# Optimization experiments

Hardware: AMD Instinct MI355X
Metric: run time of the kernel (lower is better)

Reference implementation:

```python
import jax, jax.numpy as jnp
import numpy as np

H = W = 32
C = 384
NH = 12
HEAD = C // NH
SCALE = HEAD ** -0.5
WS = 8            # window size
SS = 4            # shift size
N = WS * WS       # tokens per window (64)
NW = (H // WS) * (W // WS)  # windows per image (16)
HIDDEN = 4 * C
EPS = 1e-5
SQRT_2_OVER_PI = float(np.sqrt(2.0 / np.pi))


def _relative_position_index():
    ch = np.arange(WS)
    coords = np.stack(np.meshgrid(ch, ch, indexing='ij')).reshape(2, -1)  # [2, N]
    rel = (coords[:, :, None] - coords[:, None, :]).transpose(1, 2, 0)    # [N, N, 2]
    rel[:, :, 0] += WS - 1
    rel[:, :, 1] += WS - 1
    rel[:, :, 0] *= 2 * WS - 1
    return rel.sum(-1)  # [N, N] int


def _attn_mask():
    img = np.zeros((H, W), np.float32)
    sl = (slice(0, -WS), slice(-WS, -SS), slice(-SS, None))
    cnt = 0
    for hs in sl:
        for ws_ in sl:
            img[hs, ws_] = cnt
            cnt += 1
    m = img.reshape(H // WS, WS, W // WS, WS).transpose(0, 2, 1, 3).reshape(-1, N)  # [nW, N]
    am = m[:, None, :] - m[:, :, None]
    return np.where(am != 0, -100.0, 0.0).astype(np.float32)  # [nW, N, N]


REL_IDX = jnp.asarray(_relative_position_index())
ATTN_MASK = jnp.asarray(_attn_mask())


def _gelu(x):
    return x * 0.5 * (1.0 + jnp.tanh(SQRT_2_OVER_PI * (x + 0.044715 * x ** 3)))


def _layernorm(x, g, b):
    mu = jnp.mean(x, axis=-1, keepdims=True)
    var = jnp.mean(jnp.square(x - mu), axis=-1, keepdims=True)
    return (x - mu) * jax.lax.rsqrt(var + EPS) * g + b


def _window_partition(x):  # [B,H,W,C] -> [B*nW, N, C]
    B = x.shape[0]
    x = x.reshape(B, H // WS, WS, W // WS, WS, C).transpose(0, 1, 3, 2, 4, 5)
    return x.reshape(-1, N, C)


def _window_reverse(w, B):  # [B*nW, N, C] -> [B,H,W,C]
    x = w.reshape(B, H // WS, W // WS, WS, WS, C).transpose(0, 1, 3, 2, 4, 5)
    return x.reshape(B, H, W, C)


def setup_inputs() -> dict:
    key = jax.random.key(0)
    ks = jax.random.split(key, 16)
    s = 0.02
    return {
        'x': jax.random.normal(ks[0], (32, H * W, C), jnp.float32),
        'norm1_g': jnp.ones((C,), jnp.float32),
        'norm1_b': jnp.zeros((C,), jnp.float32),
        'qkv_w': jax.random.normal(ks[1], (C, 3 * C), jnp.float32) * s,
        'qkv_b': jnp.zeros((3 * C,), jnp.float32),
        'rel_bias_table': jax.random.normal(ks[2], ((2 * WS - 1) ** 2, NH), jnp.float32) * s,
        'proj_w': jax.random.normal(ks[3], (C, C), jnp.float32) * s,
        'proj_b': jnp.zeros((C,), jnp.float32),
        'norm2_g': jnp.ones((C,), jnp.float32),
        'norm2_b': jnp.zeros((C,), jnp.float32),
        'fc1_w': jax.random.normal(ks[4], (C, HIDDEN), jnp.float32) * s,
        'fc1_b': jnp.zeros((HIDDEN,), jnp.float32),
        'fc2_w': jax.random.normal(ks[5], (HIDDEN, C), jnp.float32) * s,
        'fc2_b': jnp.zeros((C,), jnp.float32),
    }


def reference(x, norm1_g, norm1_b, qkv_w, qkv_b, rel_bias_table, proj_w, proj_b,
              norm2_g, norm2_b, fc1_w, fc1_b, fc2_w, fc2_b):
    B = x.shape[0]
    shortcut = x
    y = _layernorm(x, norm1_g, norm1_b).reshape(B, H, W, C)
    y = jnp.roll(y, shift=(-SS, -SS), axis=(1, 2))          # cyclic shift
    win = _window_partition(y)                               # [B*nW, N, C]

    qkv = (win @ qkv_w + qkv_b).reshape(-1, N, 3, NH, HEAD).transpose(2, 0, 3, 1, 4)
    q, k, v = qkv[0], qkv[1], qkv[2]                         # [B*nW, NH, N, HEAD]
    attn = jnp.einsum('whnd,whmd->whnm', q * SCALE, k)       # [B*nW, NH, N, N]

    bias = rel_bias_table[REL_IDX.reshape(-1)].reshape(N, N, NH).transpose(2, 0, 1)
    attn = attn + bias[None]
    attn = attn.reshape(B, NW, NH, N, N) + ATTN_MASK[None, :, None]
    attn = jax.nn.softmax(attn.reshape(-1, NH, N, N), axis=-1)

    out = jnp.einsum('whnm,whmd->wnhd', attn, v).reshape(-1, N, C)
    out = out @ proj_w + proj_b                              # [B*nW, N, C]

    y = _window_reverse(out, B)
    y = jnp.roll(y, shift=(SS, SS), axis=(1, 2)).reshape(B, H * W, C)

    x = shortcut + y                                         # drop_path is identity (eval)
    h = _layernorm(x, norm2_g, norm2_b)
    h = _gelu(h @ fc1_w + fc1_b) @ fc2_w + fc2_b
    return x + h
```

## Files before the change

kernel.cpp:

```cpp
#include <hip/hip_runtime.h>
#include <hip/hip_bf16.h>
#include <math.h>

typedef __hip_bfloat16 bf16;
typedef __attribute__((ext_vector_type(8))) short short8;
typedef __attribute__((ext_vector_type(4))) float floatx4;

static constexpr int TOK = 32768;
static constexpr int CDIM = 384;
static constexpr int HID = 1536;

__device__ __forceinline__ bf16 f2bf(float v) { return __float2bfloat16(v); }

__device__ __forceinline__ unsigned short bf_bits(float a) {
  bf16 h = __float2bfloat16(a);
  unsigned short u;
  __builtin_memcpy(&u, &h, 2);
  return u;
}
__device__ __forceinline__ unsigned pack2(float a, float b) {
  return (unsigned)bf_bits(a) | ((unsigned)bf_bits(b) << 16);
}

typedef const __attribute__((address_space(1))) unsigned gas_t;
typedef __attribute__((address_space(3))) unsigned las_t;
__device__ __forceinline__ void gload16(const bf16* g, const bf16* l) {
  __builtin_amdgcn_global_load_lds((gas_t*)g, (las_t*)l, 16, 0, 0);
}

__global__ __launch_bounds__(256) void k_convt4(
    const float* __restrict__ s0, bf16* __restrict__ d0,
    const float* __restrict__ s1, bf16* __restrict__ d1,
    const float* __restrict__ s2, bf16* __restrict__ d2,
    const float* __restrict__ s3, bf16* __restrict__ d3) {
  int tid = blockIdx.x * 256 + threadIdx.x;
  const float* src; bf16* dst; int Kd, Nd, off;
  if (tid < 442368) { src = s0; dst = d0; Kd = 384; Nd = 1152; off = tid; }
  else if (tid < 589824) { src = s1; dst = d1; Kd = 384; Nd = 384; off = tid - 442368; }
  else if (tid < 1179648) { src = s2; dst = d2; Kd = 384; Nd = 1536; off = tid - 589824; }
  else { src = s3; dst = d3; Kd = 1536; Nd = 384; off = tid - 1179648; }
  int k = off / Nd, n = off - k * Nd;
  dst[(size_t)n * Kd + k] = f2bf(src[off]);
}

__global__ __launch_bounds__(256) void k_ln1(const float* __restrict__ x,
                                             const float* __restrict__ g,
                                             const float* __restrict__ b,
                                             bf16* __restrict__ out) {
  int wt = blockIdx.x * 4 + (threadIdx.x >> 6);
  int lane = threadIdx.x & 63;
  int win = wt >> 6, ntok = wt & 63;
  int bimg = win >> 4, wi = win & 15;
  int sh = (((wi >> 2) << 3) + (ntok >> 3) + 4) & 31;
  int sw = (((wi & 3) << 3) + (ntok & 7) + 4) & 31;
  const float* xr = x + ((size_t)bimg * 1024 + sh * 32 + sw) * CDIM;
  float v[6]; float s = 0.f, ss = 0.f;
#pragma unroll
  for (int j = 0; j < 6; ++j) {
    float t = xr[j * 64 + lane];
    v[j] = t; s += t; ss += t * t;
  }
#pragma unroll
  for (int off = 32; off > 0; off >>= 1) {
    s += __shfl_xor(s, off, 64);
    ss += __shfl_xor(ss, off, 64);
  }
  float mu = s * (1.f / 384.f);
  float var = ss * (1.f / 384.f) - mu * mu;
  float rs = rsqrtf(var + 1e-5f);
  bf16* orow = out + (size_t)wt * CDIM;
#pragma unroll
  for (int j = 0; j < 6; ++j) {
    int c = j * 64 + lane;
    orow[c] = f2bf((v[j] - mu) * rs * g[c] + b[c]);
  }
}

__global__ __launch_bounds__(256) void k_ln2(const float* __restrict__ x1,
                                             const float* __restrict__ g,
                                             const float* __restrict__ b,
                                             bf16* __restrict__ out) {
  int t = blockIdx.x * 4 + (threadIdx.x >> 6);
  int lane = threadIdx.x & 63;
  const float* xr = x1 + (size_t)t * CDIM;
  float v[6]; float s = 0.f, ss = 0.f;
#pragma unroll
  for (int j = 0; j < 6; ++j) {
    float q = xr[j * 64 + lane];
    v[j] = q; s += q; ss += q * q;
  }
#pragma unroll
  for (int off = 32; off > 0; off >>= 1) {
    s += __shfl_xor(s, off, 64);
    ss += __shfl_xor(ss, off, 64);
  }
  float mu = s * (1.f / 384.f);
  float var = ss * (1.f / 384.f) - mu * mu;
  float rs = rsqrtf(var + 1e-5f);
  bf16* orow = out + (size_t)t * CDIM;
#pragma unroll
  for (int j = 0; j < 6; ++j) {
    int c = j * 64 + lane;
    orow[c] = f2bf((v[j] - mu) * rs * g[c] + b[c]);
  }
}

template <int K, int EPI, int NT>
__global__ __launch_bounds__(256) void k_gemm(const bf16* __restrict__ A,
                                              const bf16* __restrict__ Bt,
                                              const float* __restrict__ bias,
                                              const float* __restrict__ extra,
                                              void* __restrict__ outp) {
  __shared__ __attribute__((aligned(16))) char pool[49152];
  bf16* A0 = (bf16*)pool;
  bf16* B0 = (bf16*)(pool + 8192);
  bf16* A1 = (bf16*)(pool + 16384);
  bf16* B1 = (bf16*)(pool + 24576);
  bf16* A2 = (bf16*)(pool + 32768);
  bf16* B2 = (bf16*)(pool + 40960);

  const int tid = threadIdx.x;
  const int wv = tid >> 6, lane = tid & 63;

  const int flat = blockIdx.x;
  const int xcd = flat & 7;
  const int idx = flat >> 3;
  const int rpx = (gridDim.x >> 3) / NT;
  const int cb = idx % NT;
  const int rb = idx / NT;
  const int mblk = (xcd * rpx + rb) * 128, nblk = cb * 128;

  const int srow = lane >> 3;
  const int sc = (lane & 7) ^ srow;
  const int srow2 = 2 * srow + (sc >> 2);
  const int gco = (sc & 3) * 8;
  const bf16* gaw = A + (size_t)(mblk + wv * 32 + srow2) * K + gco;
  const bf16* gbw = Bt + (size_t)(nblk + wv * 32 + srow2) * K + gco;
  bf16* lA0 = A0 + wv * 1024; bf16* lB0 = B0 + wv * 1024;
  bf16* lA1 = A1 + wv * 1024; bf16* lB1 = B1 + wv * 1024;
  bf16* lA2 = A2 + wv * 1024; bf16* lB2 = B2 + wv * 1024;

  const int wr = wv >> 1, wc = wv & 1;
  const int mr = lane & 15, q = lane >> 4;
  const int slot8 = ((((mr & 1) << 2) | q) ^ (mr >> 1)) * 8;
  const int faOff = (wr * 32 + (mr >> 1)) * 64 + slot8;
  const int fbOff = (wc * 32 + (mr >> 1)) * 64 + slot8;

  floatx4 acc[4][4];
#pragma unroll
  for (int i = 0; i < 4; ++i)
#pragma unroll
    for (int j = 0; j < 4; ++j) acc[i][j] = floatx4{0.f, 0.f, 0.f, 0.f};

#define VM4() asm volatile("s_waitcnt vmcnt(4)" ::: "memory")
#define VM0() asm volatile("s_waitcnt vmcnt(0)" ::: "memory")
#define BAR() __builtin_amdgcn_s_barrier()

#define STAGE(LA, LB, KOFF) do { \
    gload16(gaw + (KOFF), (LA)); \
    gload16(gaw + (KOFF) + 16 * K, (LA) + 512); \
    gload16(gbw + (KOFF), (LB)); \
    gload16(gbw + (KOFF) + 16 * K, (LB) + 512); \
  } while (0)

#define COMPUTE(ABASE, BBASE) do { \
    short8 a_[4], b_[4]; \
    _Pragma("unroll") \
    for (int mt = 0; mt < 4; ++mt) a_[mt] = *(const short8*)((ABASE) + faOff + mt * 512); \
    _Pragma("unroll") \
    for (int nt = 0; nt < 4; ++nt) b_[nt] = *(const short8*)((BBASE) + fbOff + nt * 512); \
    _Pragma("unroll") \
    for (int mt = 0; mt < 4; ++mt) \
      _Pragma("unroll") \
      for (int nt = 0; nt < 4; ++nt) \
        acc[mt][nt] = __builtin_amdgcn_mfma_f32_16x16x32_bf16(a_[mt], b_[nt], acc[mt][nt], 0, 0, 0); \
  } while (0)

  STAGE(lA0, lB0, 0);
  STAGE(lA1, lB1, 32);
  for (int k0 = 0; k0 < K - 96; k0 += 96) {
    VM4(); BAR(); STAGE(lA2, lB2, k0 + 64);  COMPUTE(A0, B0);
    VM4(); BAR(); STAGE(lA0, lB0, k0 + 96);  COMPUTE(A1, B1);
    VM4(); BAR(); STAGE(lA1, lB1, k0 + 128); COMPUTE(A2, B2);
  }
  VM4(); BAR(); STAGE(lA2, lB2, K - 32); COMPUTE(A0, B0);
  VM4(); BAR();                          COMPUTE(A1, B1);
  VM0(); BAR();                          COMPUTE(A2, B2);
#undef STAGE
#undef COMPUTE
#undef VM4
#undef VM0
#undef BAR

  __syncthreads();
  float* epsw = (float*)pool + wv * (16 * 68);
  const int rr = lane >> 2, c0 = (lane & 3) * 16;
#pragma unroll
  for (int mt = 0; mt < 4; ++mt) {
#pragma unroll
    for (int nt = 0; nt < 4; ++nt)
#pragma unroll
      for (int r = 0; r < 4; ++r)
        epsw[(q * 4 + r) * 68 + nt * 16 + mr] = acc[mt][nt][r];
    float v[16];
#pragma unroll
    for (int j = 0; j < 4; ++j) {
      float4 t = *(const float4*)&epsw[rr * 68 + c0 + j * 4];
      v[j * 4 + 0] = t.x; v[j * 4 + 1] = t.y; v[j * 4 + 2] = t.z; v[j * 4 + 3] = t.w;
    }
    const int grow = mblk + wr * 64 + mt * 16 + rr;
    const int gcol = nblk + wc * 64 + c0;

    if constexpr (EPI == 0) {
      int win = grow >> 6, ntok = grow & 63;
      int s = gcol / 384;
      int rem = gcol - s * 384;
      int h = rem >> 5, d0 = rem & 31;
      bf16* op = (bf16*)outp + (((size_t)s * 512 + win) * 12 + h) * 2048 + ntok * 32 + d0;
      uint4 pk;
      float bv[16];
#pragma unroll
      for (int j = 0; j < 16; ++j) bv[j] = v[j] + bias[gcol + j];
      pk.x = pack2(bv[0], bv[1]); pk.y = pack2(bv[2], bv[3]);
      pk.z = pack2(bv[4], bv[5]); pk.w = pack2(bv[6], bv[7]);
      *(uint4*)op = pk;
      pk.x = pack2(bv[8], bv[9]); pk.y = pack2(bv[10], bv[11]);
      pk.z = pack2(bv[12], bv[13]); pk.w = pack2(bv[14], bv[15]);
      *(uint4*)(op + 8) = pk;
    } else if constexpr (EPI == 1) {
      int win = grow >> 6, ntok = grow & 63;
      int bimg = win >> 4, wi = win & 15;
      int hh = (((wi >> 2) << 3) + (ntok >> 3) + 4) & 31;
      int ww = (((wi & 3) << 3) + (ntok & 7) + 4) & 31;
      size_t t = (size_t)bimg * 1024 + hh * 32 + ww;
      float* op = (float*)outp + t * CDIM + gcol;
      const float* xr = extra + t * CDIM + gcol;
#pragma unroll
      for (int j = 0; j < 4; ++j) {
        float4 xv = *(const float4*)(xr + j * 4);
        float4 ov;
        ov.x = xv.x + v[j * 4 + 0] + bias[gcol + j * 4 + 0];
        ov.y = xv.y + v[j * 4 + 1] + bias[gcol + j * 4 + 1];
        ov.z = xv.z + v[j * 4 + 2] + bias[gcol + j * 4 + 2];
        ov.w = xv.w + v[j * 4 + 3] + bias[gcol + j * 4 + 3];
        *(float4*)(op + j * 4) = ov;
      }
    } else if constexpr (EPI == 2) {
      float gv[16];
#pragma unroll
      for (int j = 0; j < 16; ++j) {
        float z = v[j] + bias[gcol + j];
        float u = 0.7978845608028654f * (z + 0.044715f * z * z * z);
        gv[j] = z / (1.f + __expf(-2.f * u));
      }
      bf16* op = (bf16*)outp + (size_t)grow * HID + gcol;
      uint4 pk;
      pk.x = pack2(gv[0], gv[1]); pk.y = pack2(gv[2], gv[3]);
      pk.z = pack2(gv[4], gv[5]); pk.w = pack2(gv[6], gv[7]);
      *(uint4*)op = pk;
      pk.x = pack2(gv[8], gv[9]); pk.y = pack2(gv[10], gv[11]);
      pk.z = pack2(gv[12], gv[13]); pk.w = pack2(gv[14], gv[15]);
      *(uint4*)(op + 8) = pk;
    } else {
      float* op = (float*)outp + (size_t)grow * CDIM + gcol;
      const float* xr = extra + (size_t)grow * CDIM + gcol;
#pragma unroll
      for (int j = 0; j < 4; ++j) {
        float4 xv = *(const float4*)(xr + j * 4);
        float4 ov;
        ov.x = xv.x + v[j * 4 + 0] + bias[gcol + j * 4 + 0];
        ov.y = xv.y + v[j * 4 + 1] + bias[gcol + j * 4 + 1];
        ov.z = xv.z + v[j * 4 + 2] + bias[gcol + j * 4 + 2];
        ov.w = xv.w + v[j * 4 + 3] + bias[gcol + j * 4 + 3];
        *(float4*)(op + j * 4) = ov;
      }
    }
  }
}

__global__ __launch_bounds__(64) void k_attn(const bf16* __restrict__ qkv,
                                             const float* __restrict__ tblg,
                                             bf16* __restrict__ out) {
  __shared__ __attribute__((aligned(16))) char pool[16384];
  bf16* Qs = (bf16*)pool;
  bf16* Ks = (bf16*)(pool + 5120);
  bf16* Ps = (bf16*)pool;
  float* Os = (float*)pool;
  bf16* Vt = (bf16*)(pool + 10240);
  unsigned long long* msk = (unsigned long long*)(pool + 14848);
  float* tbl = (float*)(pool + 15360);

  const int bid = blockIdx.x;
  const int win = bid / 12, head = bid - win * 12;
  const int lane = threadIdx.x;
  const int q = lane >> 4, mr = lane & 15;

  for (int i = lane; i < 225; i += 64) tbl[i] = tblg[i * 12 + head];

  size_t base = ((size_t)win * 12 + head) * 2048 + lane * 32;
  const uint4* qp = (const uint4*)(qkv + base);
  const uint4* kp = (const uint4*)(qkv + (size_t)12582912 + base);
  const uint4* vp = (const uint4*)(qkv + (size_t)25165824 + base);
#pragma unroll
  for (int i = 0; i < 4; ++i) *(uint4*)(Qs + lane * 40 + i * 8) = qp[i];
#pragma unroll
  for (int i = 0; i < 4; ++i) *(uint4*)(Ks + lane * 40 + i * 8) = kp[i];
  {
    union { uint4 u[4]; unsigned short h[32]; } vv;
#pragma unroll
    for (int i = 0; i < 4; ++i) vv.u[i] = vp[i];
    unsigned short* VtU = (unsigned short*)Vt;
#pragma unroll
    for (int d = 0; d < 32; ++d) VtU[d * 72 + lane] = vv.h[d];
  }
  {
    int wi = win & 15;
    int ri = lane >> 3, ci = lane & 7;
    int rh = ((wi >> 2) << 3) + ri, rw = ((wi & 3) << 3) + ci;
    int rid = (rh < 24 ? 0 : (rh < 28 ? 1 : 2)) * 3 + (rw < 24 ? 0 : (rw < 28 ? 1 : 2));
    unsigned long long m = 0;
#pragma unroll
    for (int v = 0; v < 9; ++v) {
      unsigned long long bb = __ballot(rid == v);
      if (rid == v) m = bb;
    }
    msk[lane] = m;
  }

  floatx4 sac[4][4];
#pragma unroll
  for (int i = 0; i < 4; ++i)
#pragma unroll
    for (int j = 0; j < 4; ++j) sac[i][j] = floatx4{0.f, 0.f, 0.f, 0.f};
  {
    short8 af[4], bf[4];
#pragma unroll
    for (int t = 0; t < 4; ++t) af[t] = *(const short8*)(Qs + (t * 16 + mr) * 40 + q * 8);
#pragma unroll
    for (int t = 0; t < 4; ++t) bf[t] = *(const short8*)(Ks + (t * 16 + mr) * 40 + q * 8);
#pragma unroll
    for (int mt = 0; mt < 4; ++mt)
#pragma unroll
      for (int nt = 0; nt < 4; ++nt)
        sac[mt][nt] = __builtin_amdgcn_mfma_f32_16x16x32_bf16(af[mt], bf[nt], sac[mt][nt], 0, 0, 0);
  }

  float psum[4][4];
#pragma unroll
  for (int mt = 0; mt < 4; ++mt)
#pragma unroll
    for (int r = 0; r < 4; ++r) psum[mt][r] = 0.f;
#pragma unroll
  for (int mt = 0; mt < 4; ++mt) {
#pragma unroll
    for (int r = 0; r < 4; ++r) {
      const int i = mt * 16 + q * 4 + r;
      const unsigned long long mrow = msk[i];
      const int bi = (i >> 3) * 15 + (i & 7);
#pragma unroll
      for (int nt = 0; nt < 4; ++nt) {
        const int j = nt * 16 + mr;
        const int idx = bi + 112 - (j >> 3) * 15 - (j & 7);
        float val = sac[mt][nt][r] * 0.17677669529663687f + tbl[idx];
        float p = __expf(val);
        p = ((mrow >> j) & 1ull) ? p : 0.f;
        psum[mt][r] += p;
        Ps[i * 72 + j] = f2bf(p);
      }
    }
  }
  float inv[4][4];
#pragma unroll
  for (int mt = 0; mt < 4; ++mt)
#pragma unroll
    for (int r = 0; r < 4; ++r) {
      float s = psum[mt][r];
      s += __shfl_xor(s, 1, 64);
      s += __shfl_xor(s, 2, 64);
      s += __shfl_xor(s, 4, 64);
      s += __shfl_xor(s, 8, 64);
      inv[mt][r] = 1.f / s;
    }

  floatx4 oac[4][2];
#pragma unroll
  for (int i = 0; i < 4; ++i)
#pragma unroll
    for (int j = 0; j < 2; ++j) oac[i][j] = floatx4{0.f, 0.f, 0.f, 0.f};
#pragma unroll
  for (int kk = 0; kk < 2; ++kk) {
    short8 ap[4], bv[2];
#pragma unroll
    for (int mt = 0; mt < 4; ++mt)
      ap[mt] = *(const short8*)(Ps + (mt * 16 + mr) * 72 + kk * 32 + q * 8);
#pragma unroll
    for (int nt = 0; nt < 2; ++nt)
      bv[nt] = *(const short8*)(Vt + (nt * 16 + mr) * 72 + kk * 32 + q * 8);
#pragma unroll
    for (int mt = 0; mt < 4; ++mt)
#pragma unroll
      for (int nt = 0; nt < 2; ++nt)
        oac[mt][nt] = __builtin_amdgcn_mfma_f32_16x16x32_bf16(ap[mt], bv[nt], oac[mt][nt], 0, 0, 0);
  }

#pragma unroll
  for (int mt = 0; mt < 4; ++mt)
#pragma unroll
    for (int nt = 0; nt < 2; ++nt)
#pragma unroll
      for (int r = 0; r < 4; ++r)
        Os[(mt * 16 + q * 4 + r) * 40 + nt * 16 + mr] = oac[mt][nt][r] * inv[mt][r];
  float ov[32];
#pragma unroll
  for (int c = 0; c < 8; ++c) {
    const int cc = c ^ (lane & 7);
    float4 t = *(const float4*)(Os + lane * 40 + cc * 4);
    ov[cc * 4 + 0] = t.x; ov[cc * 4 + 1] = t.y;
    ov[cc * 4 + 2] = t.z; ov[cc * 4 + 3] = t.w;
  }
  uint4* o4 = (uint4*)(out + ((size_t)win * 64 + lane) * CDIM + head * 32);
#pragma unroll
  for (int i = 0; i < 4; ++i) {
    uint4 pk;
    pk.x = pack2(ov[i * 8 + 0], ov[i * 8 + 1]);
    pk.y = pack2(ov[i * 8 + 2], ov[i * 8 + 3]);
    pk.z = pack2(ov[i * 8 + 4], ov[i * 8 + 5]);
    pk.w = pack2(ov[i * 8 + 6], ov[i * 8 + 7]);
    o4[i] = pk;
  }
}

extern "C" void kernel_launch(void* const* d_in, const int* in_sizes, int n_in,
                              void* d_out, int out_size, void* d_ws, size_t ws_size,
                              hipStream_t stream) {
  const float* x = (const float*)d_in[0];
  const float* n1g = (const float*)d_in[1];
  const float* n1b = (const float*)d_in[2];
  const float* qkv_w = (const float*)d_in[3];
  const float* qkv_b = (const float*)d_in[4];
  const float* reltbl = (const float*)d_in[5];
  const float* proj_w = (const float*)d_in[6];
  const float* proj_b = (const float*)d_in[7];
  const float* n2g = (const float*)d_in[8];
  const float* n2b = (const float*)d_in[9];
  const float* fc1_w = (const float*)d_in[10];
  const float* fc1_b = (const float*)d_in[11];
  const float* fc2_w = (const float*)d_in[12];
  const float* fc2_b = (const float*)d_in[13];
  float* out = (float*)d_out;

  char* p = (char*)d_ws;
  bf16* w_qkv_t = (bf16*)p;  p += (size_t)442368 * 2;
  bf16* w_proj_t = (bf16*)p; p += (size_t)147456 * 2;
  bf16* w_fc1_t = (bf16*)p;  p += (size_t)589824 * 2;
  bf16* w_fc2_t = (bf16*)p;  p += (size_t)589824 * 2;
  bf16* bufA = (bf16*)p;     p += (size_t)12582912 * 2;
  bf16* qkvb = (bf16*)p;     p += (size_t)37748736 * 2;
  bf16* attno = (bf16*)p;    p += (size_t)12582912 * 2;
  float* x1 = (float*)p;     p += (size_t)12582912 * 4;
  bf16* hidden = qkvb;

  k_convt4<<<dim3(6912), dim3(256), 0, stream>>>(qkv_w, w_qkv_t, proj_w, w_proj_t,
                                                 fc1_w, w_fc1_t, fc2_w, w_fc2_t);

  k_ln1<<<dim3(8192), dim3(256), 0, stream>>>(x, n1g, n1b, bufA);
  k_gemm<384, 0, 9><<<dim3(9 * 256), dim3(256), 0, stream>>>(bufA, w_qkv_t, qkv_b, nullptr, qkvb);
  k_attn<<<dim3(6144), dim3(64), 0, stream>>>(qkvb, reltbl, attno);
  k_gemm<384, 1, 3><<<dim3(3 * 256), dim3(256), 0, stream>>>(attno, w_proj_t, proj_b, x, x1);
  k_ln2<<<dim3(8192), dim3(256), 0, stream>>>(x1, n2g, n2b, bufA);
  k_gemm<384, 2, 12><<<dim3(12 * 256), dim3(256), 0, stream>>>(bufA, w_fc1_t, fc1_b, nullptr, hidden);
  k_gemm<1536, 3, 3><<<dim3(3 * 256), dim3(256), 0, stream>>>(hidden, w_fc2_t, fc2_b, x1, out);
}
```

Baseline: 398.6 us.

## Enlarge GEMM tiles to 256x128 with 8 waves and simplify GELU epilogue

The GEMM kernel moves from 256-thread 128x128 tiles to 512-thread 256x128 tiles, so each B tile in shared memory is reused across twice as many rows. Shared memory grows to 72KB with the B buffers relocated, each wave issues one fewer global load per stage, and the wait count drops to match. The GELU epilogue is rewritten as one fused exponent argument with a hardware reciprocal instead of a divide. The bigger block raises LDS use per block, which may lower occupancy, and halves the grid size.

```diff
diff --git a/kernel.cpp b/kernel.cpp
--- a/kernel.cpp
+++ b/kernel.cpp
@@ -106,18 +106,18 @@
 }
 
 template <int K, int EPI, int NT>
-__global__ __launch_bounds__(256) void k_gemm(const bf16* __restrict__ A,
-                                              const bf16* __restrict__ Bt,
-                                              const float* __restrict__ bias,
-                                              const float* __restrict__ extra,
-                                              void* __restrict__ outp) {
-  __shared__ __attribute__((aligned(16))) char pool[49152];
+__global__ __launch_bounds__(512, 4) void k_gemm(const bf16* __restrict__ A,
+                                                 const bf16* __restrict__ Bt,
+                                                 const float* __restrict__ bias,
+                                                 const float* __restrict__ extra,
+                                                 void* __restrict__ outp) {
+  __shared__ __attribute__((aligned(16))) char pool[73728];
   bf16* A0 = (bf16*)pool;
-  bf16* B0 = (bf16*)(pool + 8192);
   bf16* A1 = (bf16*)(pool + 16384);
-  bf16* B1 = (bf16*)(pool + 24576);
   bf16* A2 = (bf16*)(pool + 32768);
-  bf16* B2 = (bf16*)(pool + 40960);
+  bf16* B0 = (bf16*)(pool + 49152);
+  bf16* B1 = (bf16*)(pool + 57344);
+  bf16* B2 = (bf16*)(pool + 65536);
 
   const int tid = threadIdx.x;
   const int wv = tid >> 6, lane = tid & 63;
@@ -128,17 +128,16 @@
   const int rpx = (gridDim.x >> 3) / NT;
   const int cb = idx % NT;
   const int rb = idx / NT;
-  const int mblk = (xcd * rpx + rb) * 128, nblk = cb * 128;
+  const int mblk = (xcd * rpx + rb) * 256, nblk = cb * 128;
 
   const int srow = lane >> 3;
   const int sc = (lane & 7) ^ srow;
   const int srow2 = 2 * srow + (sc >> 2);
   const int gco = (sc & 3) * 8;
   const bf16* gaw = A + (size_t)(mblk + wv * 32 + srow2) * K + gco;
-  const bf16* gbw = Bt + (size_t)(nblk + wv * 32 + srow2) * K + gco;
-  bf16* lA0 = A0 + wv * 1024; bf16* lB0 = B0 + wv * 1024;
-  bf16* lA1 = A1 + wv * 1024; bf16* lB1 = B1 + wv * 1024;
-  bf16* lA2 = A2 + wv * 1024; bf16* lB2 = B2 + wv * 1024;
+  const bf16* gbw = Bt + (size_t)(nblk + wv * 16 + srow2) * K + gco;
+  const int lAo = wv * 1024;
+  const int lBo = wv * 512;
 
   const int wr = wv >> 1, wc = wv & 1;
   const int mr = lane & 15, q = lane >> 4;
@@ -152,15 +151,14 @@
 #pragma unroll
     for (int j = 0; j < 4; ++j) acc[i][j] = floatx4{0.f, 0.f, 0.f, 0.f};
 
-#define VM4() asm volatile("s_waitcnt vmcnt(4)" ::: "memory")
+#define VM3() asm volatile("s_waitcnt vmcnt(3)" ::: "memory")
 #define VM0() asm volatile("s_waitcnt vmcnt(0)" ::: "memory")
 #define BAR() __builtin_amdgcn_s_barrier()
 
 #define STAGE(LA, LB, KOFF) do { \
-    gload16(gaw + (KOFF), (LA)); \
-    gload16(gaw + (KOFF) + 16 * K, (LA) + 512); \
-    gload16(gbw + (KOFF), (LB)); \
-    gload16(gbw + (KOFF) + 16 * K, (LB) + 512); \
+    gload16(gaw + (KOFF), (LA) + lAo); \
+    gload16(gaw + (KOFF) + 16 * K, (LA) + lAo + 512); \
+    gload16(gbw + (KOFF), (LB) + lBo); \
   } while (0)
 
 #define COMPUTE(ABASE, BBASE) do { \
@@ -176,24 +174,24 @@
         acc[mt][nt] = __builtin_amdgcn_mfma_f32_16x16x32_bf16(a_[mt], b_[nt], acc[mt][nt], 0, 0, 0); \
   } while (0)
 
-  STAGE(lA0, lB0, 0);
-  STAGE(lA1, lB1, 32);
+  STAGE(A0, B0, 0);
+  STAGE(A1, B1, 32);
   for (int k0 = 0; k0 < K - 96; k0 += 96) {
-    VM4(); BAR(); STAGE(lA2, lB2, k0 + 64);  COMPUTE(A0, B0);
-    VM4(); BAR(); STAGE(lA0, lB0, k0 + 96);  COMPUTE(A1, B1);
-    VM4(); BAR(); STAGE(lA1, lB1, k0 + 128); COMPUTE(A2, B2);
-  }
-  VM4(); BAR(); STAGE(lA2, lB2, K - 32); COMPUTE(A0, B0);
-  VM4(); BAR();                          COMPUTE(A1, B1);
-  VM0(); BAR();                          COMPUTE(A2, B2);
+    VM3(); BAR(); STAGE(A2, B2, k0 + 64);  COMPUTE(A0, B0);
+    VM3(); BAR(); STAGE(A0, B0, k0 + 96);  COMPUTE(A1, B1);
+    VM3(); BAR(); STAGE(A1, B1, k0 + 128); COMPUTE(A2, B2);
+  }
+  VM3(); BAR(); STAGE(A2, B2, K - 32); COMPUTE(A0, B0);
+  VM3(); BAR();                        COMPUTE(A1, B1);
+  VM0(); BAR();                        COMPUTE(A2, B2);
 #undef STAGE
 #undef COMPUTE
-#undef VM4
+#undef VM3
 #undef VM0
 #undef BAR
 
   __syncthreads();
-  float* epsw = (float*)pool + wv * (16 * 68);
+  float* epsw = (float*)(pool + wv * 4352);
   const int rr = lane >> 2, c0 = (lane & 3) * 16;
 #pragma unroll
   for (int mt = 0; mt < 4; ++mt) {
@@ -250,8 +248,10 @@
 #pragma unroll
       for (int j = 0; j < 16; ++j) {
         float z = v[j] + bias[gcol + j];
-        float u = 0.7978845608028654f * (z + 0.044715f * z * z * z);
-        gv[j] = z / (1.f + __expf(-2.f * u));
+        float t2 = z * z;
+        float c = __builtin_fmaf(t2, -0.0713548162f, -1.5957691216f);
+        float e = __expf(z * c);
+        gv[j] = z * __builtin_amdgcn_rcpf(1.f + e);
       }
       bf16* op = (bf16*)outp + (size_t)grow * HID + gcol;
       uint4 pk;
@@ -464,10 +464,10 @@
                                                  fc1_w, w_fc1_t, fc2_w, w_fc2_t);
 
   k_ln1<<<dim3(8192), dim3(256), 0, stream>>>(x, n1g, n1b, bufA);
-  k_gemm<384, 0, 9><<<dim3(9 * 256), dim3(256), 0, stream>>>(bufA, w_qkv_t, qkv_b, nullptr, qkvb);
+  k_gemm<384, 0, 9><<<dim3(128 * 9), dim3(512), 0, stream>>>(bufA, w_qkv_t, qkv_b, nullptr, qkvb);
   k_attn<<<dim3(6144), dim3(64), 0, stream>>>(qkvb, reltbl, attno);
-  k_gemm<384, 1, 3><<<dim3(3 * 256), dim3(256), 0, stream>>>(attno, w_proj_t, proj_b, x, x1);
+  k_gemm<384, 1, 3><<<dim3(128 * 3), dim3(512), 0, stream>>>(attno, w_proj_t, proj_b, x, x1);
   k_ln2<<<dim3(8192), dim3(256), 0, stream>>>(x1, n2g, n2b, bufA);
-  k_gemm<384, 2, 12><<<dim3(12 * 256), dim3(256), 0, stream>>>(bufA, w_fc1_t, fc1_b, nullptr, hidden);
-  k_gemm<1536, 3, 3><<<dim3(3 * 256), dim3(256), 0, stream>>>(hidden, w_fc2_t, fc2_b, x1, out);
-}
+  k_gemm<384, 2, 12><<<dim3(128 * 12), dim3(512), 0, stream>>>(bufA, w_fc1_t, fc1_b, nullptr, hidden);
+  k_gemm<1536, 3, 3><<<dim3(128 * 3), dim3(512), 0, stream>>>(hidden, w_fc2_t, fc2_b, x1, out);
+}
```

Result: slower. 418.9 us (+5.1%).

## Fuse MLP fc1, GELU and fc2 into one kernel keeping hidden in LDS

Applied to the files above, without the earlier changes.

Replaces the separate fc1 (GELU epilogue) and fc2 GEMM launches with one k_mlp kernel. Each 512-thread block owns 128 tokens and walks the hidden dimension in 128-wide chunks: it computes fc1, applies GELU into a bf16 LDS tile, then accumulates into fc2. This avoids writing and re-reading the 32768x1536 bf16 hidden tensor in global memory. In exchange it launches only 256 blocks, uses 128KB of LDS per block and holds a large register accumulator, which may limit occupancy and latency hiding.

```diff
diff --git a/kernel.cpp b/kernel.cpp
--- a/kernel.cpp
+++ b/kernel.cpp
@@ -245,37 +245,200 @@
         ov.w = xv.w + v[j * 4 + 3] + bias[gcol + j * 4 + 3];
         *(float4*)(op + j * 4) = ov;
       }
-    } else if constexpr (EPI == 2) {
-      float gv[16];
-#pragma unroll
-      for (int j = 0; j < 16; ++j) {
-        float z = v[j] + bias[gcol + j];
-        float u = 0.7978845608028654f * (z + 0.044715f * z * z * z);
-        gv[j] = z / (1.f + __expf(-2.f * u));
-      }
-      bf16* op = (bf16*)outp + (size_t)grow * HID + gcol;
-      uint4 pk;
-      pk.x = pack2(gv[0], gv[1]); pk.y = pack2(gv[2], gv[3]);
-      pk.z = pack2(gv[4], gv[5]); pk.w = pack2(gv[6], gv[7]);
-      *(uint4*)op = pk;
-      pk.x = pack2(gv[8], gv[9]); pk.y = pack2(gv[10], gv[11]);
-      pk.z = pack2(gv[12], gv[13]); pk.w = pack2(gv[14], gv[15]);
-      *(uint4*)(op + 8) = pk;
-    } else {
-      float* op = (float*)outp + (size_t)grow * CDIM + gcol;
-      const float* xr = extra + (size_t)grow * CDIM + gcol;
-#pragma unroll
-      for (int j = 0; j < 4; ++j) {
-        float4 xv = *(const float4*)(xr + j * 4);
-        float4 ov;
-        ov.x = xv.x + v[j * 4 + 0] + bias[gcol + j * 4 + 0];
-        ov.y = xv.y + v[j * 4 + 1] + bias[gcol + j * 4 + 1];
-        ov.z = xv.z + v[j * 4 + 2] + bias[gcol + j * 4 + 2];
-        ov.w = xv.w + v[j * 4 + 3] + bias[gcol + j * 4 + 3];
-        *(float4*)(op + j * 4) = ov;
+    }
+  }
+}
+
+__global__ __launch_bounds__(512, 2) void k_mlp(const bf16* __restrict__ A,
+                                                const bf16* __restrict__ W1t,
+                                                const bf16* __restrict__ W2t,
+                                                const float* __restrict__ b1,
+                                                const float* __restrict__ b2,
+                                                const float* __restrict__ x1,
+                                                float* __restrict__ out) {
+  __shared__ __attribute__((aligned(16))) char pool[131072];
+  bf16* A0 = (bf16*)pool;
+  bf16* A1 = (bf16*)(pool + 8192);
+  bf16* A2 = (bf16*)(pool + 16384);
+  bf16* W10 = (bf16*)(pool + 24576);
+  bf16* W11 = (bf16*)(pool + 32768);
+  bf16* W12 = (bf16*)(pool + 40960);
+  bf16* hs = (bf16*)(pool + 49152);
+  bf16* W2sA = (bf16*)(pool + 81920);
+  bf16* W2sB = (bf16*)(pool + 106496);
+
+  const int tid = threadIdx.x;
+  const int wv = tid >> 6, lane = tid & 63;
+  const int mblk = blockIdx.x * 128;
+
+  const int srow = lane >> 3;
+  const int sc = (lane & 7) ^ srow;
+  const int srow2 = 2 * srow + (sc >> 2);
+  const int gco = (sc & 3) * 8;
+
+  const bf16* ga = A + (size_t)(mblk + wv * 16 + srow2) * 384 + gco;
+  const bf16* g1 = W1t + (size_t)(wv * 16 + srow2) * 384 + gco;
+  const bf16* g2 = W2t + (size_t)(wv * 48 + srow2) * 1536 + gco;
+
+  const int wr1 = wv >> 2, wc1 = wv & 3;
+  const int mr = lane & 15, q = lane >> 4;
+  const int slot8 = ((((mr & 1) << 2) | q) ^ (mr >> 1)) * 8;
+  const int faOff1 = (wr1 * 32 + (mr >> 1)) * 64 + slot8;
+  const int fbOff1 = (wc1 * 16 + (mr >> 1)) * 64 + slot8;
+  const int fbOff2 = (wc1 * 48 + (mr >> 1)) * 64 + slot8;
+  const size_t hb = (size_t)(wr1 * 64 + mr) * 128;
+  int px[4];
+#pragma unroll
+  for (int kk = 0; kk < 4; ++kk)
+    px[kk] = (((kk & 2) << 2) | ((((kk & 1) << 2) | q) ^ (mr & 7))) * 8;
+
+  floatx4 acc1[4][2];
+  floatx4 acc2[4][6];
+#pragma unroll
+  for (int i = 0; i < 4; ++i) {
+#pragma unroll
+    for (int j = 0; j < 2; ++j) acc1[i][j] = floatx4{0.f, 0.f, 0.f, 0.f};
+#pragma unroll
+    for (int j = 0; j < 6; ++j) acc2[i][j] = floatx4{0.f, 0.f, 0.f, 0.f};
+  }
+
+#define VMW(N) asm volatile("s_waitcnt vmcnt(" #N ")" ::: "memory")
+#define BARR() __builtin_amdgcn_s_barrier()
+#define ST(ABUF, WBUF, G1P, KO) do { \
+    gload16(ga + (KO), (ABUF) + wv * 512); \
+    gload16((G1P) + (KO), (WBUF) + wv * 512); \
+  } while (0)
+#define STW2(BUF, KK) do { \
+    _Pragma("unroll") \
+    for (int g = 0; g < 3; ++g) \
+      gload16(g2 + (KK) * 32 + (size_t)g * 16 * 1536, (BUF) + wv * 1536 + g * 512); \
+  } while (0)
+#define C1(AB, WB) do { \
+    short8 a_[4], b_[2]; \
+    _Pragma("unroll") \
+    for (int mt = 0; mt < 4; ++mt) a_[mt] = *(const short8*)((AB) + faOff1 + mt * 512); \
+    b_[0] = *(const short8*)((WB) + fbOff1); \
+    b_[1] = *(const short8*)((WB) + fbOff1 + 512); \
+    _Pragma("unroll") \
+    for (int mt = 0; mt < 4; ++mt) \
+      _Pragma("unroll") \
+      for (int nt = 0; nt < 2; ++nt) \
+        acc1[mt][nt] = __builtin_amdgcn_mfma_f32_16x16x32_bf16(a_[mt], b_[nt], acc1[mt][nt], 0, 0, 0); \
+  } while (0)
+#define C2(BUF, KK) do { \
+    short8 ha[4], wb[6]; \
+    _Pragma("unroll") \
+    for (int mt = 0; mt < 4; ++mt) \
+      ha[mt] = *(const short8*)(hs + hb + mt * 2048 + px[KK]); \
+    _Pragma("unroll") \
+    for (int nt = 0; nt < 6; ++nt) \
+      wb[nt] = *(const short8*)((BUF) + fbOff2 + nt * 512); \
+    _Pragma("unroll") \
+    for (int mt = 0; mt < 4; ++mt) \
+      _Pragma("unroll") \
+      for (int nt = 0; nt < 6; ++nt) \
+        acc2[mt][nt] = __builtin_amdgcn_mfma_f32_16x16x32_bf16(ha[mt], wb[nt], acc2[mt][nt], 0, 0, 0); \
+  } while (0)
+
+  ST(A0, W10, g1, 0);
+  ST(A1, W11, g1, 32);
+
+  for (int ci = 0; ci < 12; ++ci) {
+    BARR();
+    const int cb = ci * 128;
+    float bb0 = b1[cb + wc1 * 32 + mr];
+    float bb1 = b1[cb + wc1 * 32 + 16 + mr];
+    STW2(W2sA, 0);
+
+    const bf16* g1n = g1 + 49152;
+    VMW(5); BARR(); ST(A2, W12, g1, 64);   C1(A0, W10);
+    VMW(5); BARR(); ST(A0, W10, g1, 96);   C1(A1, W11);
+    VMW(2); BARR(); ST(A1, W11, g1, 128);  C1(A2, W12);
+    VMW(2); BARR(); ST(A2, W12, g1, 160);  C1(A0, W10);
+    VMW(2); BARR(); ST(A0, W10, g1, 192);  C1(A1, W11);
+    VMW(2); BARR(); ST(A1, W11, g1, 224);  C1(A2, W12);
+    VMW(2); BARR(); ST(A2, W12, g1, 256);  C1(A0, W10);
+    VMW(2); BARR(); ST(A0, W10, g1, 288);  C1(A1, W11);
+    VMW(2); BARR(); ST(A1, W11, g1, 320);  C1(A2, W12);
+    VMW(2); BARR(); ST(A2, W12, g1, 352);  C1(A0, W10);
+    VMW(2); BARR(); ST(A0, W10, g1n, 0);   C1(A1, W11);
+    VMW(2); BARR(); ST(A1, W11, g1n, 32);  C1(A2, W12);
+
+#pragma unroll
+    for (int mt = 0; mt < 4; ++mt) {
+      const int tokb = wr1 * 64 + mt * 16 + q * 4;
+#pragma unroll
+      for (int nt = 0; nt < 2; ++nt) {
+        const float bb = nt ? bb1 : bb0;
+        const int sw = wc1 * 4 + nt * 2 + (mr >> 3);
+        const int s8 = sw & 8, s7 = sw & 7;
+#pragma unroll
+        for (int r = 0; r < 4; ++r) {
+          float z = acc1[mt][nt][r] + bb;
+          float t2 = z * z;
+          float cp = __builtin_fmaf(t2, -0.0713548162f, -1.5957691216f);
+          float e = __expf(z * cp);
+          float gl = z * __builtin_amdgcn_rcpf(1.f + e);
+          const int t7 = ((q & 1) << 2) | r;
+          hs[(size_t)(tokb + r) * 128 + (s8 | (s7 ^ t7)) * 8 + (mr & 7)] = f2bf(gl);
+        }
+        acc1[mt][nt] = floatx4{0.f, 0.f, 0.f, 0.f};
       }
     }
-  }
+    __syncthreads();
+
+    STW2(W2sB, 1);
+    C2(W2sA, 0);
+    BARR();
+    STW2(W2sA, 2);
+    VMW(3); BARR();
+    C2(W2sB, 1);
+    BARR();
+    STW2(W2sB, 3);
+    VMW(3); BARR();
+    C2(W2sA, 2);
+    VMW(0); BARR();
+    C2(W2sB, 3);
+
+    g1 += 49152;
+    g2 += 128;
+  }
+#undef ST
+#undef STW2
+#undef C1
+#undef C2
+
+  VMW(0);
+  __syncthreads();
+
+  float* epsw = (float*)(pool + wv * 6400);
+  const int rr = lane >> 2, c4 = (lane & 3) * 24;
+#pragma unroll
+  for (int mt = 0; mt < 4; ++mt) {
+#pragma unroll
+    for (int nt = 0; nt < 6; ++nt)
+#pragma unroll
+      for (int r = 0; r < 4; ++r)
+        epsw[(q * 4 + r) * 100 + nt * 16 + mr] = acc2[mt][nt][r];
+    const int grow = mblk + wr1 * 64 + mt * 16 + rr;
+    const int gcol = wc1 * 96 + c4;
+    const float* xr = x1 + (size_t)grow * 384 + gcol;
+    float* op = out + (size_t)grow * 384 + gcol;
+#pragma unroll
+    for (int j = 0; j < 6; ++j) {
+      float4 t = *(const float4*)&epsw[rr * 100 + c4 + j * 4];
+      float4 xv = *(const float4*)(xr + j * 4);
+      float4 bv = *(const float4*)&b2[gcol + j * 4];
+      float4 ov;
+      ov.x = xv.x + t.x + bv.x;
+      ov.y = xv.y + t.y + bv.y;
+      ov.z = xv.z + t.z + bv.z;
+      ov.w = xv.w + t.w + bv.w;
+      *(float4*)(op + j * 4) = ov;
+    }
+  }
+#undef VMW
+#undef BARR
 }
 
 __global__ __launch_bounds__(64) void k_attn(const bf16* __restrict__ qkv,
@@ -458,7 +621,6 @@
   bf16* qkvb = (bf16*)p;     p += (size_t)37748736 * 2;
   bf16* attno = (bf16*)p;    p += (size_t)12582912 * 2;
   float* x1 = (float*)p;     p += (size_t)12582912 * 4;
-  bf16* hidden = qkvb;
 
   k_convt4<<<dim3(6912), dim3(256), 0, stream>>>(qkv_w, w_qkv_t, proj_w, w_proj_t,
                                                  fc1_w, w_fc1_t, fc2_w, w_fc2_t);
@@ -468,6 +630,5 @@
   k_attn<<<dim3(6144), dim3(64), 0, stream>>>(qkvb, reltbl, attno);
   k_gemm<384, 1, 3><<<dim3(3 * 256), dim3(256), 0, stream>>>(attno, w_proj_t, proj_b, x, x1);
   k_ln2<<<dim3(8192), dim3(256), 0, stream>>>(x1, n2g, n2b, bufA);
-  k_gemm<384, 2, 12><<<dim3(12 * 256), dim3(256), 0, stream>>>(bufA, w_fc1_t, fc1_b, nullptr, hidden);
-  k_gemm<1536, 3, 3><<<dim3(3 * 256), dim3(256), 0, stream>>>(hidden, w_fc2_t, fc2_b, x1, out);
-}
+  k_mlp<<<dim3(256), dim3(512), 0, stream>>>(bufA, w_fc1_t, w_fc2_t, fc1_b, fc2_b, x1, out);
+}
```

Result: faster. 387.4 us (-2.8%).
